# Kernel optimization log

Measured on AMD Instinct MI355X. Metric: run time of the kernel, lower is better.

The kernel has to match this reference:

```python
import jax, jax.numpy as jnp
import numpy as np

B, S, H = 4, 512, 1024
E, K, I = 8, 2, 2048

def setup_inputs() -> dict:
    key = jax.random.key(0)
    k1, k2, k3, k4, k5 = jax.random.split(key, 5)
    scale_h = 1.0 / np.sqrt(H)
    scale_i = 1.0 / np.sqrt(I)
    return {
        "hidden_states": jax.random.normal(k1, (B, S, H), dtype=jnp.float32),
        "router_w": jax.random.normal(k2, (E, H), dtype=jnp.float32) * scale_h,
        "w_gate": jax.random.normal(k3, (E, H, I), dtype=jnp.float32) * scale_h,
        "w_up": jax.random.normal(k4, (E, H, I), dtype=jnp.float32) * scale_h,
        "w_down": jax.random.normal(k5, (E, I, H), dtype=jnp.float32) * scale_i,
    }

def reference(hidden_states, router_w, w_gate, w_up, w_down):
    b, s, h = hidden_states.shape
    x = hidden_states.reshape(-1, h)              # [T, H] tokens
    T = x.shape[0]

    # ---- RouterTopK: fp32 linear -> softmax over all experts -> top-k ----
    router_logits = x.astype(jnp.float32) @ router_w.T          # [T, E]
    probs = jax.nn.softmax(router_logits, axis=-1)               # [T, E]
    top_vals, top_idx = jax.lax.top_k(probs, K)                  # [T, K]

    # normalize_top_k_affinities (norm_topk_prob=True)
    top_vals = top_vals / jnp.sum(top_vals, axis=-1, keepdims=True)

    # scatter normalized affinities into a dense [T, E] combine matrix
    aff = jnp.zeros((T, E), dtype=x.dtype).at[jnp.arange(T)[:, None], top_idx].set(top_vals.astype(x.dtype))

    # ---- ExpertMLPs: GLU (swiglu) per expert, combine weighted by affinity ----
    # Dense-per-expert computation; non-selected experts contribute 0 via aff.
    gate = jnp.einsum('th,ehi->eti', x, w_gate)                  # [E, T, I]
    up = jnp.einsum('th,ehi->eti', x, w_up)                      # [E, T, I]
    act = jax.nn.silu(gate) * up                                 # [E, T, I]
    expert_out = jnp.einsum('eti,eih->eth', act, w_down)         # [E, T, H]
    out = jnp.einsum('eth,te->th', expert_out, aff)              # [T, H]

    # _reduce_output: all-reduce over TP/world group -> identity single-device
    return out.reshape(b, s, h)
```

## Files before the change

kernel.cpp:

```cpp
#include <hip/hip_runtime.h>
#include <hip/hip_bf16.h>

#define T_TOK 2048
#define H_DIM 1024
#define E_N   8
#define I_DIM 2048
#define GW    4096

#define NT_MAX 40
#define SLOTS  5120

typedef unsigned short u16;
typedef unsigned int   u32;
typedef __bf16 bf16_t;
typedef bf16_t bf16x8 __attribute__((ext_vector_type(8)));
typedef u16    u16x8  __attribute__((ext_vector_type(8)));
typedef u16    u16x4  __attribute__((ext_vector_type(4)));
typedef float  f32x16 __attribute__((ext_vector_type(16)));

#define MFMA32 __builtin_amdgcn_mfma_f32_32x32x16_bf16

__device__ __forceinline__ u16 bfbits(float f) {
    bf16_t b = (bf16_t)f;
    return __builtin_bit_cast(u16, b);
}
__device__ __forceinline__ float bf2f(u16 u) {
    u32 x = ((u32)u) << 16;
    return __builtin_bit_cast(float, x);
}

__device__ __forceinline__ void gload_lds16(const void* g, void* l) {
    __builtin_amdgcn_global_load_lds(
        (const __attribute__((address_space(1))) void*)g,
        (__attribute__((address_space(3))) void*)l, 16, 0, 0);
}

__device__ __forceinline__ int tile_off(int n, int kb) {
    return n * 64 + ((kb ^ ((n >> 1) & 7)) << 3);
}
__device__ __forceinline__ int a_off(int row, int kslot) {
    return row * 64 + ((kslot ^ (row & 7)) << 3);
}

__global__ __launch_bounds__(256) void router_k(
    const float* __restrict__ x, const float* __restrict__ rw,
    int* __restrict__ cnt, int* __restrict__ tok,
    int4* __restrict__ invA, float2* __restrict__ invW,
    u16* __restrict__ xbf)
{
    int wid = threadIdx.x >> 6, lane = threadIdx.x & 63;
    int t = blockIdx.x * 4 + wid;
    const float* xr = x + (size_t)t * H_DIM;
    u16* xbr = xbf + (size_t)t * H_DIM;

    float acc[E_N];
#pragma unroll
    for (int e = 0; e < E_N; e++) acc[e] = 0.f;
#pragma unroll
    for (int j = 0; j < H_DIM / 256; j++) {
        int o = lane * 4 + j * 256;
        float4 xv = *reinterpret_cast<const float4*>(xr + o);
        u16x4 p;
        p[0] = bfbits(xv.x); p[1] = bfbits(xv.y); p[2] = bfbits(xv.z); p[3] = bfbits(xv.w);
        *reinterpret_cast<u16x4*>(xbr + o) = p;
#pragma unroll
        for (int e = 0; e < E_N; e++) {
            float4 wv = *reinterpret_cast<const float4*>(rw + e * H_DIM + o);
            acc[e] += xv.x * wv.x + xv.y * wv.y + xv.z * wv.z + xv.w * wv.w;
        }
    }
#pragma unroll
    for (int e = 0; e < E_N; e++) {
        float v = acc[e];
        for (int off = 32; off; off >>= 1) v += __shfl_xor(v, off);
        acc[e] = v;
    }
    if (lane == 0) {
        int i0 = 0; float m0 = acc[0];
#pragma unroll
        for (int e = 1; e < E_N; e++) if (acc[e] > m0) { m0 = acc[e]; i0 = e; }
        int i1 = -1; float m1 = -INFINITY;
#pragma unroll
        for (int e = 0; e < E_N; e++) if (e != i0 && acc[e] > m1) { m1 = acc[e]; i1 = e; }
        float w0 = 1.f / (1.f + expf(m1 - m0));
        float w1 = 1.f - w0;
        int p0 = atomicAdd(&cnt[i0], 1);
        tok[i0 * T_TOK + p0] = t;
        int p1 = atomicAdd(&cnt[i1], 1);
        tok[i1 * T_TOK + p1] = t;
        invA[t] = make_int4(i0, p0, i1, p1);
        invW[t] = make_float2(w0, w1);
    }
}

__global__ void prefix_k(const int* __restrict__ cnt, int* __restrict__ offs_pad,
                         int* __restrict__ tile_e, int* __restrict__ tile_row0,
                         int* __restrict__ ntiles)
{
    if (threadIdx.x == 0) {
        int s = 0, nt = 0;
        for (int e = 0; e < E_N; e++) {
            offs_pad[e] = s;
            int c = cnt[e];
            int t = (c + 127) >> 7;
            for (int i = 0; i < t; i++) { tile_e[nt] = e; tile_row0[nt] = i * 128; nt++; }
            s += t * 128;
        }
        offs_pad[E_N] = s;
        *ntiles = nt;
    }
}

__global__ __launch_bounds__(256, 3) void gu_k(
    const u16* __restrict__ xbf, const float* __restrict__ wg, const float* __restrict__ wu,
    const int* __restrict__ cnt, const int* __restrict__ offs_pad,
    const int* __restrict__ tile_e, const int* __restrict__ tile_row0,
    const int* __restrict__ ntiles, const int* __restrict__ tok,
    u16* __restrict__ gbuf)
{
    int q = gridDim.x >> 3;
    int phys = blockIdx.x;
    int logical = (phys & 7) * q + (phys >> 3);
    int tb = logical % NT_MAX;
    int p  = logical / NT_MAX;
    if (tb >= *ntiles) return;
    int e = tile_e[tb], row0 = tile_row0[tb];
    int cntE = cnt[e];
    int slot0 = offs_pad[e] + row0;
    int n0 = p * 128;
    int mat  = n0 >> 11;
    int coln = n0 & 2047;

    __shared__ u16 AS[2][8192], BS[8192];

    int tid = threadIdx.x;
    int lane = tid & 63, wid = tid >> 6;
    int wm = wid >> 1, wn = wid & 1;
    int l31 = lane & 31, lh = lane >> 5;

    const u16* asrc[4];
#pragma unroll
    for (int i = 0; i < 4; i++) {
        int row = (wid * 4 + i) * 8 + (lane >> 3);
        int rc = (row0 + row < cntE) ? (row0 + row) : (cntE - 1);
        asrc[i] = xbf + (size_t)tok[e * T_TOK + rc] * H_DIM
                  + (((lane & 7) ^ ((lane >> 3) & 7)) << 3);
    }
    int s0 = wid * 2048;

    int bn = tid & 127;
    int khalf = tid >> 7;
    const float* wsrc = (mat ? wu : wg) + (size_t)e * H_DIM * I_DIM + coln + bn;

    float v[32];

#define BLOAD(t) { \
    _Pragma("unroll") \
    for (int j = 0; j < 32; j++) \
        v[j] = wsrc[(size_t)((t) * 64 + khalf * 32 + j) * I_DIM]; }

#define BWRITE() { \
    _Pragma("unroll") \
    for (int jb = 0; jb < 4; jb++) { \
        u16x8 pk; \
        _Pragma("unroll") \
        for (int jj = 0; jj < 8; jj++) pk[jj] = bfbits(v[jb * 8 + jj]); \
        *reinterpret_cast<u16x8*>(&BS[tile_off(bn, khalf * 4 + jb)]) = pk; } }

#define ASTAGE(nbuf, t) { \
    _Pragma("unroll") \
    for (int i = 0; i < 4; i++) \
        gload_lds16(asrc[i] + (size_t)(t) * 64, &AS[nbuf][s0 + i * 512]); }

    f32x16 acc[2][2];
#pragma unroll
    for (int a = 0; a < 2; a++)
#pragma unroll
        for (int b = 0; b < 2; b++) acc[a][b] = (f32x16)0.f;

#define CLUSTER(bufi) { \
    _Pragma("unroll") \
    for (int ks = 0; ks < 4; ks++) { \
        bf16x8 af[2], bfr[2]; \
        _Pragma("unroll") \
        for (int mf = 0; mf < 2; mf++) \
            af[mf] = *reinterpret_cast<const bf16x8*>(&AS[bufi][a_off(wm * 64 + mf * 32 + l31, ks * 2 + lh)]); \
        _Pragma("unroll") \
        for (int nf = 0; nf < 2; nf++) \
            bfr[nf] = *reinterpret_cast<const bf16x8*>(&BS[tile_off(wn * 64 + nf * 32 + l31, ks * 2 + lh)]); \
        _Pragma("unroll") \
        for (int mf = 0; mf < 2; mf++) \
            _Pragma("unroll") \
            for (int nf = 0; nf < 2; nf++) \
                acc[mf][nf] = MFMA32(af[mf], bfr[nf], acc[mf][nf], 0, 0, 0); } }

    ASTAGE(0, 0);
    __builtin_amdgcn_sched_barrier(0);
    BLOAD(0);
    __builtin_amdgcn_sched_barrier(0);
    BWRITE();
    __builtin_amdgcn_sched_barrier(0);
    asm volatile("s_waitcnt vmcnt(0) lgkmcnt(0)" ::: "memory");
    __builtin_amdgcn_s_barrier();
    __builtin_amdgcn_sched_barrier(0);

    for (int t = 0; t < 16; t++) {
        int abuf = t & 1;
        bool more = (t + 1) < 16;
        if (more) {
            ASTAGE(abuf ^ 1, t + 1);
            __builtin_amdgcn_sched_barrier(0);
            BLOAD(t + 1);
            __builtin_amdgcn_sched_barrier(0);
        }
        CLUSTER(abuf);
        __builtin_amdgcn_sched_barrier(0);
        if (more) {
            __builtin_amdgcn_s_barrier();
            __builtin_amdgcn_sched_barrier(0);
            BWRITE();
            __builtin_amdgcn_sched_barrier(0);
            asm volatile("s_waitcnt vmcnt(0) lgkmcnt(0)" ::: "memory");
            __builtin_amdgcn_s_barrier();
            __builtin_amdgcn_sched_barrier(0);
        }
    }
#undef BLOAD
#undef BWRITE
#undef ASTAGE
#undef CLUSTER

#pragma unroll
    for (int mf = 0; mf < 2; mf++)
#pragma unroll
        for (int nf = 0; nf < 2; nf++) {
            int col = n0 + wn * 64 + nf * 32 + l31;
#pragma unroll
            for (int r = 0; r < 16; r++) {
                int rl = wm * 64 + mf * 32 + (r & 3) + 8 * (r >> 2) + 4 * lh;
                gbuf[(size_t)(slot0 + rl) * GW + col] = bfbits(acc[mf][nf][r]);
            }
        }
}

__global__ __launch_bounds__(256) void act_k(const u16* __restrict__ gbuf,
                                             u16* __restrict__ act)
{
    int s = blockIdx.x;
    int i = threadIdx.x * 8;
    u16x8 g8 = *reinterpret_cast<const u16x8*>(&gbuf[(size_t)s * GW + i]);
    u16x8 u8 = *reinterpret_cast<const u16x8*>(&gbuf[(size_t)s * GW + 2048 + i]);
    u16x8 o;
#pragma unroll
    for (int j = 0; j < 8; j++) {
        float g = bf2f(g8[j]);
        float u = bf2f(u8[j]);
        o[j] = bfbits(g / (1.f + expf(-g)) * u);
    }
    *reinterpret_cast<u16x8*>(&act[(size_t)s * I_DIM + i]) = o;
}

__global__ __launch_bounds__(256, 3) void down_k(
    const u16* __restrict__ act, const float* __restrict__ wd,
    const int* __restrict__ cnt, const int* __restrict__ offs_pad,
    const int* __restrict__ tile_e, const int* __restrict__ tile_row0,
    const int* __restrict__ ntiles, const int* __restrict__ tok,
    u16* __restrict__ dbuf)
{
    int q = gridDim.x >> 3;
    int phys = blockIdx.x;
    int logical = (phys & 7) * q + (phys >> 3);
    int tb = logical % NT_MAX;
    int rest = logical / NT_MAX;
    int p  = rest & 7;
    int kh = rest >> 3;
    if (tb >= *ntiles) return;
    int e = tile_e[tb], row0 = tile_row0[tb];
    int slot0 = offs_pad[e] + row0;
    int h0 = p * 128;

    __shared__ u16 AS[2][8192], BS[8192];

    int tid = threadIdx.x;
    int lane = tid & 63, wid = tid >> 6;
    int wm = wid >> 1, wn = wid & 1;
    int l31 = lane & 31, lh = lane >> 5;

    const u16* asrc[4];
#pragma unroll
    for (int i = 0; i < 4; i++) {
        int row = (wid * 4 + i) * 8 + (lane >> 3);
        asrc[i] = act + (size_t)(slot0 + row) * I_DIM + kh * 1024
                  + (((lane & 7) ^ ((lane >> 3) & 7)) << 3);
    }
    int s0 = wid * 2048;

    int bn = tid & 127;
    int khalf = tid >> 7;
    const float* dsrc = wd + ((size_t)e * I_DIM + kh * 1024) * H_DIM + h0 + bn;

    float v[32];

#define BLOAD(t) { \
    _Pragma("unroll") \
    for (int j = 0; j < 32; j++) \
        v[j] = dsrc[(size_t)((t) * 64 + khalf * 32 + j) * H_DIM]; }

#define BWRITE() { \
    _Pragma("unroll") \
    for (int jb = 0; jb < 4; jb++) { \
        u16x8 pk; \
        _Pragma("unroll") \
        for (int jj = 0; jj < 8; jj++) pk[jj] = bfbits(v[jb * 8 + jj]); \
        *reinterpret_cast<u16x8*>(&BS[tile_off(bn, khalf * 4 + jb)]) = pk; } }

#define ASTAGE(nbuf, t) { \
    _Pragma("unroll") \
    for (int i = 0; i < 4; i++) \
        gload_lds16(asrc[i] + (size_t)(t) * 64, &AS[nbuf][s0 + i * 512]); }

    f32x16 acc[2][2];
#pragma unroll
    for (int a = 0; a < 2; a++)
#pragma unroll
        for (int b = 0; b < 2; b++) acc[a][b] = (f32x16)0.f;

#define CLUSTER(bufi) { \
    _Pragma("unroll") \
    for (int ks = 0; ks < 4; ks++) { \
        bf16x8 af[2], bfr[2]; \
        _Pragma("unroll") \
        for (int mf = 0; mf < 2; mf++) \
            af[mf] = *reinterpret_cast<const bf16x8*>(&AS[bufi][a_off(wm * 64 + mf * 32 + l31, ks * 2 + lh)]); \
        _Pragma("unroll") \
        for (int nf = 0; nf < 2; nf++) \
            bfr[nf] = *reinterpret_cast<const bf16x8*>(&BS[tile_off(wn * 64 + nf * 32 + l31, ks * 2 + lh)]); \
        _Pragma("unroll") \
        for (int mf = 0; mf < 2; mf++) \
            _Pragma("unroll") \
            for (int nf = 0; nf < 2; nf++) \
                acc[mf][nf] = MFMA32(af[mf], bfr[nf], acc[mf][nf], 0, 0, 0); } }

    ASTAGE(0, 0);
    __builtin_amdgcn_sched_barrier(0);
    BLOAD(0);
    __builtin_amdgcn_sched_barrier(0);
    BWRITE();
    __builtin_amdgcn_sched_barrier(0);
    asm volatile("s_waitcnt vmcnt(0) lgkmcnt(0)" ::: "memory");
    __builtin_amdgcn_s_barrier();
    __builtin_amdgcn_sched_barrier(0);

    for (int t = 0; t < 16; t++) {
        int abuf = t & 1;
        bool more = (t + 1) < 16;
        if (more) {
            ASTAGE(abuf ^ 1, t + 1);
            __builtin_amdgcn_sched_barrier(0);
            BLOAD(t + 1);
            __builtin_amdgcn_sched_barrier(0);
        }
        CLUSTER(abuf);
        __builtin_amdgcn_sched_barrier(0);
        if (more) {
            __builtin_amdgcn_s_barrier();
            __builtin_amdgcn_sched_barrier(0);
            BWRITE();
            __builtin_amdgcn_sched_barrier(0);
            asm volatile("s_waitcnt vmcnt(0) lgkmcnt(0)" ::: "memory");
            __builtin_amdgcn_s_barrier();
            __builtin_amdgcn_sched_barrier(0);
        }
    }
#undef BLOAD
#undef BWRITE
#undef ASTAGE
#undef CLUSTER

#pragma unroll
    for (int mf = 0; mf < 2; mf++)
#pragma unroll
        for (int nf = 0; nf < 2; nf++) {
            int col = h0 + wn * 64 + nf * 32 + l31;
#pragma unroll
            for (int r = 0; r < 16; r++) {
                int rl = wm * 64 + mf * 32 + (r & 3) + 8 * (r >> 2) + 4 * lh;
                dbuf[(size_t)(kh * SLOTS + slot0 + rl) * H_DIM + col] = bfbits(acc[mf][nf][r]);
            }
        }
}

__global__ __launch_bounds__(256) void gather_k(
    const u16* __restrict__ dbuf, const int4* __restrict__ invA,
    const float2* __restrict__ invW, const int* __restrict__ offs_pad,
    float* __restrict__ out)
{
    int t = blockIdx.x;
    int h = threadIdx.x * 4;
    int4 ia = invA[t];
    float2 w = invW[t];
    int s0 = offs_pad[ia.x] + ia.y;
    int s1 = offs_pad[ia.z] + ia.w;

    u16x4 a0 = *reinterpret_cast<const u16x4*>(&dbuf[(size_t)s0 * H_DIM + h]);
    u16x4 a1 = *reinterpret_cast<const u16x4*>(&dbuf[(size_t)(SLOTS + s0) * H_DIM + h]);
    u16x4 b0 = *reinterpret_cast<const u16x4*>(&dbuf[(size_t)s1 * H_DIM + h]);
    u16x4 b1 = *reinterpret_cast<const u16x4*>(&dbuf[(size_t)(SLOTS + s1) * H_DIM + h]);

    float4 o;
    float* op = &o.x;
#pragma unroll
    for (int j = 0; j < 4; j++)
        op[j] = w.x * (bf2f(a0[j]) + bf2f(a1[j])) + w.y * (bf2f(b0[j]) + bf2f(b1[j]));
    *reinterpret_cast<float4*>(&out[(size_t)t * H_DIM + h]) = o;
}

extern "C" void kernel_launch(void* const* d_in, const int* in_sizes, int n_in,
                              void* d_out, int out_size, void* d_ws, size_t ws_size,
                              hipStream_t stream)
{
    const float* x  = (const float*)d_in[0];
    const float* rw = (const float*)d_in[1];
    const float* wg = (const float*)d_in[2];
    const float* wu = (const float*)d_in[3];
    const float* wd = (const float*)d_in[4];
    float* out = (float*)d_out;

    char* ws = (char*)d_ws;
    int*    cnt       = (int*)(ws);
    int*    ntiles    = (int*)(ws + 32);
    int*    offs_pad  = (int*)(ws + 64);
    int*    tile_e    = (int*)(ws + 256);
    int*    tile_row0 = (int*)(ws + 512);
    int*    tok       = (int*)(ws + 64 * 1024);
    int4*   invA      = (int4*)(ws + 160 * 1024);
    float2* invW      = (float2*)(ws + 200 * 1024);
    u16*    xbf       = (u16*)(ws + 256 * 1024);
    u16*    act       = (u16*)(ws + 5ull * 1024 * 1024);
    u16*    gbuf      = (u16*)(ws + 26ull * 1024 * 1024);
    u16*    dbuf      = (u16*)(ws + 67ull * 1024 * 1024);

    size_t need = 88ull * 1024 * 1024;
    if (ws_size < need) return;

    hipMemsetAsync(cnt, 0, 32, stream);

    router_k<<<T_TOK / 4, 256, 0, stream>>>(x, rw, cnt, tok, invA, invW, xbf);
    prefix_k<<<1, 64, 0, stream>>>(cnt, offs_pad, tile_e, tile_row0, ntiles);
    gu_k<<<NT_MAX * (GW / 128), 256, 0, stream>>>(
        xbf, wg, wu, cnt, offs_pad, tile_e, tile_row0, ntiles, tok, gbuf);
    act_k<<<SLOTS, 256, 0, stream>>>(gbuf, act);
    down_k<<<NT_MAX * (H_DIM / 128) * 2, 256, 0, stream>>>(
        act, wd, cnt, offs_pad, tile_e, tile_row0, ntiles, tok, dbuf);
    gather_k<<<T_TOK, 256, 0, stream>>>(dbuf, invA, invW, offs_pad, out);
}
```

Baseline: 206.9 us.

## Use 256-row M tiles with 512-thread blocks and 4-way K split in down projection

Measured after the change: 211.6 us. 2.3% more time.

```diff
diff --git a/kernel.cpp b/kernel.cpp
--- a/kernel.cpp
+++ b/kernel.cpp
@@ -7,8 +7,8 @@
 #define I_DIM 2048
 #define GW    4096
 
-#define NT_MAX 40
-#define SLOTS  5120
+#define NT_MAX 24
+#define SLOTS  6144
 
 typedef unsigned short u16;
 typedef unsigned int   u32;
@@ -19,6 +19,7 @@
 typedef float  f32x16 __attribute__((ext_vector_type(16)));
 
 #define MFMA32 __builtin_amdgcn_mfma_f32_32x32x16_bf16
+#define SB()   __builtin_amdgcn_sched_barrier(0)
 
 __device__ __forceinline__ u16 bfbits(float f) {
     bf16_t b = (bf16_t)f;
@@ -102,16 +103,16 @@
         for (int e = 0; e < E_N; e++) {
             offs_pad[e] = s;
             int c = cnt[e];
-            int t = (c + 127) >> 7;
-            for (int i = 0; i < t; i++) { tile_e[nt] = e; tile_row0[nt] = i * 128; nt++; }
-            s += t * 128;
+            int t = (c + 255) >> 8;
+            for (int i = 0; i < t; i++) { tile_e[nt] = e; tile_row0[nt] = i * 256; nt++; }
+            s += t * 256;
         }
         offs_pad[E_N] = s;
         *ntiles = nt;
     }
 }
 
-__global__ __launch_bounds__(256, 3) void gu_k(
+__global__ __launch_bounds__(512, 4) void gu_k(
     const u16* __restrict__ xbf, const float* __restrict__ wg, const float* __restrict__ wu,
     const int* __restrict__ cnt, const int* __restrict__ offs_pad,
     const int* __restrict__ tile_e, const int* __restrict__ tile_row0,
@@ -131,7 +132,7 @@
     int mat  = n0 >> 11;
     int coln = n0 & 2047;
 
-    __shared__ u16 AS[2][8192], BS[8192];
+    __shared__ u16 AS[2][16384], BS[8192];
 
     int tid = threadIdx.x;
     int lane = tid & 63, wid = tid >> 6;
@@ -141,7 +142,7 @@
     const u16* asrc[4];
 #pragma unroll
     for (int i = 0; i < 4; i++) {
-        int row = (wid * 4 + i) * 8 + (lane >> 3);
+        int row = wid * 32 + i * 8 + (lane >> 3);
         int rc = (row0 + row < cntE) ? (row0 + row) : (cntE - 1);
         asrc[i] = xbf + (size_t)tok[e * T_TOK + rc] * H_DIM
                   + (((lane & 7) ^ ((lane >> 3) & 7)) << 3);
@@ -149,23 +150,23 @@
     int s0 = wid * 2048;
 
     int bn = tid & 127;
-    int khalf = tid >> 7;
+    int kq = tid >> 7;
     const float* wsrc = (mat ? wu : wg) + (size_t)e * H_DIM * I_DIM + coln + bn;
 
-    float v[32];
+    float v[16];
 
 #define BLOAD(t) { \
     _Pragma("unroll") \
-    for (int j = 0; j < 32; j++) \
-        v[j] = wsrc[(size_t)((t) * 64 + khalf * 32 + j) * I_DIM]; }
+    for (int j = 0; j < 16; j++) \
+        v[j] = wsrc[(size_t)((t) * 64 + kq * 16 + j) * I_DIM]; }
 
 #define BWRITE() { \
     _Pragma("unroll") \
-    for (int jb = 0; jb < 4; jb++) { \
+    for (int jb = 0; jb < 2; jb++) { \
         u16x8 pk; \
         _Pragma("unroll") \
         for (int jj = 0; jj < 8; jj++) pk[jj] = bfbits(v[jb * 8 + jj]); \
-        *reinterpret_cast<u16x8*>(&BS[tile_off(bn, khalf * 4 + jb)]) = pk; } }
+        *reinterpret_cast<u16x8*>(&BS[tile_off(bn, kq * 2 + jb)]) = pk; } }
 
 #define ASTAGE(nbuf, t) { \
     _Pragma("unroll") \
@@ -195,34 +196,34 @@
                 acc[mf][nf] = MFMA32(af[mf], bfr[nf], acc[mf][nf], 0, 0, 0); } }
 
     ASTAGE(0, 0);
-    __builtin_amdgcn_sched_barrier(0);
+    SB();
     BLOAD(0);
-    __builtin_amdgcn_sched_barrier(0);
+    SB();
     BWRITE();
-    __builtin_amdgcn_sched_barrier(0);
+    SB();
     asm volatile("s_waitcnt vmcnt(0) lgkmcnt(0)" ::: "memory");
     __builtin_amdgcn_s_barrier();
-    __builtin_amdgcn_sched_barrier(0);
+    SB();
 
     for (int t = 0; t < 16; t++) {
-        int abuf = t & 1;
+        int ab = t & 1;
         bool more = (t + 1) < 16;
         if (more) {
-            ASTAGE(abuf ^ 1, t + 1);
-            __builtin_amdgcn_sched_barrier(0);
+            ASTAGE(ab ^ 1, t + 1);
+            SB();
             BLOAD(t + 1);
-            __builtin_amdgcn_sched_barrier(0);
-        }
-        CLUSTER(abuf);
-        __builtin_amdgcn_sched_barrier(0);
+            SB();
+        }
+        CLUSTER(ab);
+        SB();
+        __builtin_amdgcn_s_barrier();
+        SB();
         if (more) {
-            __builtin_amdgcn_s_barrier();
-            __builtin_amdgcn_sched_barrier(0);
             BWRITE();
-            __builtin_amdgcn_sched_barrier(0);
+            SB();
             asm volatile("s_waitcnt vmcnt(0) lgkmcnt(0)" ::: "memory");
             __builtin_amdgcn_s_barrier();
-            __builtin_amdgcn_sched_barrier(0);
+            SB();
         }
     }
 #undef BLOAD
@@ -243,8 +244,7 @@
         }
 }
 
-__global__ __launch_bounds__(256) void act_k(const u16* __restrict__ gbuf,
-                                             u16* __restrict__ act)
+__global__ __launch_bounds__(256) void act_k(u16* __restrict__ gbuf)
 {
     int s = blockIdx.x;
     int i = threadIdx.x * 8;
@@ -257,11 +257,11 @@
         float u = bf2f(u8[j]);
         o[j] = bfbits(g / (1.f + expf(-g)) * u);
     }
-    *reinterpret_cast<u16x8*>(&act[(size_t)s * I_DIM + i]) = o;
-}
-
-__global__ __launch_bounds__(256, 3) void down_k(
-    const u16* __restrict__ act, const float* __restrict__ wd,
+    *reinterpret_cast<u16x8*>(&gbuf[(size_t)s * GW + i]) = o;
+}
+
+__global__ __launch_bounds__(512, 4) void down_k(
+    const u16* __restrict__ gbuf, const float* __restrict__ wd,
     const int* __restrict__ cnt, const int* __restrict__ offs_pad,
     const int* __restrict__ tile_e, const int* __restrict__ tile_row0,
     const int* __restrict__ ntiles, const int* __restrict__ tok,
@@ -272,14 +272,14 @@
     int logical = (phys & 7) * q + (phys >> 3);
     int tb = logical % NT_MAX;
     int rest = logical / NT_MAX;
-    int p  = rest & 7;
-    int kh = rest >> 3;
+    int p   = rest & 7;
+    int kq4 = rest >> 3;
     if (tb >= *ntiles) return;
     int e = tile_e[tb], row0 = tile_row0[tb];
     int slot0 = offs_pad[e] + row0;
     int h0 = p * 128;
 
-    __shared__ u16 AS[2][8192], BS[8192];
+    __shared__ u16 AS[2][16384], BS[8192];
 
     int tid = threadIdx.x;
     int lane = tid & 63, wid = tid >> 6;
@@ -289,30 +289,30 @@
     const u16* asrc[4];
 #pragma unroll
     for (int i = 0; i < 4; i++) {
-        int row = (wid * 4 + i) * 8 + (lane >> 3);
-        asrc[i] = act + (size_t)(slot0 + row) * I_DIM + kh * 1024
+        int row = wid * 32 + i * 8 + (lane >> 3);
+        asrc[i] = gbuf + (size_t)(slot0 + row) * GW + kq4 * 512
                   + (((lane & 7) ^ ((lane >> 3) & 7)) << 3);
     }
     int s0 = wid * 2048;
 
     int bn = tid & 127;
-    int khalf = tid >> 7;
-    const float* dsrc = wd + ((size_t)e * I_DIM + kh * 1024) * H_DIM + h0 + bn;
-
-    float v[32];
+    int kq = tid >> 7;
+    const float* dsrc = wd + ((size_t)e * I_DIM + kq4 * 512) * H_DIM + h0 + bn;
+
+    float v[16];
 
 #define BLOAD(t) { \
     _Pragma("unroll") \
-    for (int j = 0; j < 32; j++) \
-        v[j] = dsrc[(size_t)((t) * 64 + khalf * 32 + j) * H_DIM]; }
+    for (int j = 0; j < 16; j++) \
+        v[j] = dsrc[(size_t)((t) * 64 + kq * 16 + j) * H_DIM]; }
 
 #define BWRITE() { \
     _Pragma("unroll") \
-    for (int jb = 0; jb < 4; jb++) { \
+    for (int jb = 0; jb < 2; jb++) { \
         u16x8 pk; \
         _Pragma("unroll") \
         for (int jj = 0; jj < 8; jj++) pk[jj] = bfbits(v[jb * 8 + jj]); \
-        *reinterpret_cast<u16x8*>(&BS[tile_off(bn, khalf * 4 + jb)]) = pk; } }
+        *reinterpret_cast<u16x8*>(&BS[tile_off(bn, kq * 2 + jb)]) = pk; } }
 
 #define ASTAGE(nbuf, t) { \
     _Pragma("unroll") \
@@ -342,34 +342,34 @@
                 acc[mf][nf] = MFMA32(af[mf], bfr[nf], acc[mf][nf], 0, 0, 0); } }
 
     ASTAGE(0, 0);
-    __builtin_amdgcn_sched_barrier(0);
+    SB();
     BLOAD(0);
-    __builtin_amdgcn_sched_barrier(0);
+    SB();
     BWRITE();
-    __builtin_amdgcn_sched_barrier(0);
+    SB();
     asm volatile("s_waitcnt vmcnt(0) lgkmcnt(0)" ::: "memory");
     __builtin_amdgcn_s_barrier();
-    __builtin_amdgcn_sched_barrier(0);
-
-    for (int t = 0; t < 16; t++) {
-        int abuf = t & 1;
-        bool more = (t + 1) < 16;
+    SB();
+
+    for (int t = 0; t < 8; t++) {
+        int ab = t & 1;
+        bool more = (t + 1) < 8;
         if (more) {
-            ASTAGE(abuf ^ 1, t + 1);
-            __builtin_amdgcn_sched_barrier(0);
+            ASTAGE(ab ^ 1, t + 1);
+            SB();
             BLOAD(t + 1);
-            __builtin_amdgcn_sched_barrier(0);
-        }
-        CLUSTER(abuf);
-        __builtin_amdgcn_sched_barrier(0);
+            SB();
+        }
+        CLUSTER(ab);
+        SB();
+        __builtin_amdgcn_s_barrier();
+        SB();
         if (more) {
-            __builtin_amdgcn_s_barrier();
-            __builtin_amdgcn_sched_barrier(0);
             BWRITE();
-            __builtin_amdgcn_sched_barrier(0);
+            SB();
             asm volatile("s_waitcnt vmcnt(0) lgkmcnt(0)" ::: "memory");
             __builtin_amdgcn_s_barrier();
-            __builtin_amdgcn_sched_barrier(0);
+            SB();
         }
     }
 #undef BLOAD
@@ -385,7 +385,7 @@
 #pragma unroll
             for (int r = 0; r < 16; r++) {
                 int rl = wm * 64 + mf * 32 + (r & 3) + 8 * (r >> 2) + 4 * lh;
-                dbuf[(size_t)(kh * SLOTS + slot0 + rl) * H_DIM + col] = bfbits(acc[mf][nf][r]);
+                dbuf[(size_t)(kq4 * SLOTS + slot0 + rl) * H_DIM + col] = bfbits(acc[mf][nf][r]);
             }
         }
 }
@@ -402,16 +402,16 @@
     int s0 = offs_pad[ia.x] + ia.y;
     int s1 = offs_pad[ia.z] + ia.w;
 
-    u16x4 a0 = *reinterpret_cast<const u16x4*>(&dbuf[(size_t)s0 * H_DIM + h]);
-    u16x4 a1 = *reinterpret_cast<const u16x4*>(&dbuf[(size_t)(SLOTS + s0) * H_DIM + h]);
-    u16x4 b0 = *reinterpret_cast<const u16x4*>(&dbuf[(size_t)s1 * H_DIM + h]);
-    u16x4 b1 = *reinterpret_cast<const u16x4*>(&dbuf[(size_t)(SLOTS + s1) * H_DIM + h]);
-
-    float4 o;
+    float4 o = make_float4(0.f, 0.f, 0.f, 0.f);
     float* op = &o.x;
 #pragma unroll
-    for (int j = 0; j < 4; j++)
-        op[j] = w.x * (bf2f(a0[j]) + bf2f(a1[j])) + w.y * (bf2f(b0[j]) + bf2f(b1[j]));
+    for (int qk = 0; qk < 4; qk++) {
+        u16x4 a = *reinterpret_cast<const u16x4*>(&dbuf[(size_t)(qk * SLOTS + s0) * H_DIM + h]);
+        u16x4 b = *reinterpret_cast<const u16x4*>(&dbuf[(size_t)(qk * SLOTS + s1) * H_DIM + h]);
+#pragma unroll
+        for (int j = 0; j < 4; j++)
+            op[j] += w.x * bf2f(a[j]) + w.y * bf2f(b[j]);
+    }
     *reinterpret_cast<float4*>(&out[(size_t)t * H_DIM + h]) = o;
 }
 
@@ -436,21 +436,20 @@
     int4*   invA      = (int4*)(ws + 160 * 1024);
     float2* invW      = (float2*)(ws + 200 * 1024);
     u16*    xbf       = (u16*)(ws + 256 * 1024);
-    u16*    act       = (u16*)(ws + 5ull * 1024 * 1024);
-    u16*    gbuf      = (u16*)(ws + 26ull * 1024 * 1024);
-    u16*    dbuf      = (u16*)(ws + 67ull * 1024 * 1024);
-
-    size_t need = 88ull * 1024 * 1024;
+    u16*    gbuf      = (u16*)(ws + 5ull * 1024 * 1024);
+    u16*    dbuf      = (u16*)(ws + 53ull * 1024 * 1024);
+
+    size_t need = 102ull * 1024 * 1024;
     if (ws_size < need) return;
 
     hipMemsetAsync(cnt, 0, 32, stream);
 
     router_k<<<T_TOK / 4, 256, 0, stream>>>(x, rw, cnt, tok, invA, invW, xbf);
     prefix_k<<<1, 64, 0, stream>>>(cnt, offs_pad, tile_e, tile_row0, ntiles);
-    gu_k<<<NT_MAX * (GW / 128), 256, 0, stream>>>(
+    gu_k<<<NT_MAX * (GW / 128), 512, 0, stream>>>(
         xbf, wg, wu, cnt, offs_pad, tile_e, tile_row0, ntiles, tok, gbuf);
-    act_k<<<SLOTS, 256, 0, stream>>>(gbuf, act);
-    down_k<<<NT_MAX * (H_DIM / 128) * 2, 256, 0, stream>>>(
-        act, wd, cnt, offs_pad, tile_e, tile_row0, ntiles, tok, dbuf);
+    act_k<<<SLOTS, 256, 0, stream>>>(gbuf);
+    down_k<<<NT_MAX * (H_DIM / 128) * 4, 512, 0, stream>>>(
+        gbuf, wd, cnt, offs_pad, tile_e, tile_row0, ntiles, tok, dbuf);
     gather_k<<<T_TOK, 256, 0, stream>>>(dbuf, invA, invW, offs_pad, out);
 }
```
